# Kernel optimization log

Measured on AMD Instinct MI355X. Metric: run time of the kernel, lower is better.

Reference implementation:

```python
import jax, jax.numpy as jnp
import numpy as np

VOCAB = 32000
HIDDEN = 2048
NLAYERS = 6
BATCH = 512


def setup_inputs() -> dict:
    key = jax.random.key(0)
    k1, k2, k3, k4 = jax.random.split(key, 4)
    state = jax.random.normal(k1, (BATCH, HIDDEN), dtype=jnp.float32)
    token = jax.random.randint(k2, (BATCH,), 0, VOCAB, dtype=jnp.int32)
    ih = jax.random.normal(k3, (NLAYERS, VOCAB, HIDDEN), dtype=jnp.float32) * 0.02
    hh = jax.random.normal(k4, (NLAYERS, HIDDEN, HIDDEN), dtype=jnp.float32) * 0.02
    return {"state": state, "token": token, "ih": ih, "hh": hh}


def reference(state, token, ih, hh):
    # Per layer: state = tanh(state + (state @ hh[i]) * ih[i][token])
    n_layers = ih.shape[0]
    for i in range(n_layers):
        gate = ih[i][token]                  # [B, H] embedding gather
        state = jnp.tanh(state + jnp.matmul(state, hh[i]) * gate)
    return state
```

## Files before the change

kernel.cpp:

```cpp
#include <hip/hip_runtime.h>
#include <hip/hip_bf16.h>
#include <cstdint>
#include <cstddef>

#define VOCAB 32000
#define HIDDEN 2048
#define NLAYERS 6
#define BATCH 512

#define BM 64
#define BN 64
#define BK 64
#define SPLITK 4
#define KC (HIDDEN / SPLITK)
#define NT (KC / BK)
#define GEMM_BLOCKS 1024
#define TRANS_BLOCKS 1024
#define CVT_BLOCKS 1024

typedef __attribute__((ext_vector_type(8))) short bf16x8;
typedef __attribute__((ext_vector_type(4))) float f32x4;

__device__ __forceinline__ unsigned short f2bf(float f) {
  unsigned u = __builtin_bit_cast(unsigned, f);
  u += 0x7fffu + ((u >> 16) & 1u);
  return (unsigned short)(u >> 16);
}

__device__ __forceinline__ float bf2f(unsigned short h) {
  return __builtin_bit_cast(float, (unsigned)h << 16);
}

__device__ __forceinline__ float tanh_fast(float x) {
  x = fminf(15.f, fmaxf(-15.f, x));
  float e = __expf(2.f * x);
  return (e - 1.f) / (e + 1.f);
}

__device__ __forceinline__ void gload_lds16(const void* g, void* l) {
  __builtin_amdgcn_global_load_lds(
      (const __attribute__((address_space(1))) void*)g,
      (__attribute__((address_space(3))) void*)l, 16, 0, 0);
}

__device__ __forceinline__ void transpose_tile(const float* __restrict__ src_layer,
                                               unsigned short* __restrict__ dst_layer,
                                               int n0, int k0, int t,
                                               unsigned short (*tile)[72]) {
  const float* src = src_layer + (size_t)k0 * HIDDEN + n0;
  const int cr = t >> 4;
  const int cc = (t & 15) * 4;
#pragma unroll
  for (int p = 0; p < 4; ++p) {
    const int r = p * 16 + cr;
    float4 v = *(const float4*)(src + (size_t)r * HIDDEN + cc);
    tile[r][cc + 0] = f2bf(v.x);
    tile[r][cc + 1] = f2bf(v.y);
    tile[r][cc + 2] = f2bf(v.z);
    tile[r][cc + 3] = f2bf(v.w);
  }
  __syncthreads();
  const int nl = t >> 2;
  const int kk = (t & 3) * 16;
  unsigned short tmp[16] __attribute__((aligned(16)));
#pragma unroll
  for (int j = 0; j < 16; ++j) tmp[j] = tile[kk + j][nl];
  unsigned short* dst = dst_layer + (size_t)(n0 + nl) * HIDDEN + k0 + kk;
  *(uint4*)(dst) = *(const uint4*)(tmp);
  *(uint4*)(dst + 8) = *(const uint4*)(tmp + 8);
}

__global__ __launch_bounds__(256) void k_prep0(const float* __restrict__ hh0,
                                               unsigned short* __restrict__ bt0,
                                               const float* __restrict__ state,
                                               unsigned short* __restrict__ stb) {
  __shared__ unsigned short tile[64][72];
  const int wg = blockIdx.x;
  const int t = threadIdx.x;
  if (wg < TRANS_BLOCKS) {
    transpose_tile(hh0, bt0, (wg & 31) * 64, (wg >> 5) * 64, t, tile);
    return;
  }
  const int i = ((wg - TRANS_BLOCKS) * 256 + t) * 4;
  float4 v = *(const float4*)(state + i);
  union { unsigned short h[4]; uint2 u; } o;
  o.h[0] = f2bf(v.x); o.h[1] = f2bf(v.y); o.h[2] = f2bf(v.z); o.h[3] = f2bf(v.w);
  *(uint2*)(stb + i) = o.u;
}

__global__ __launch_bounds__(256, 4) void k_gemm_trans(
    const unsigned short* __restrict__ A, const unsigned short* __restrict__ Bt,
    unsigned short* __restrict__ part,
    const float* __restrict__ hhNext, unsigned short* __restrict__ btNext) {
  __shared__ __attribute__((aligned(16))) unsigned char smem[32768];
  const int t = threadIdx.x;
  const int wg = blockIdx.x;

  if (wg >= GEMM_BLOCKS) {
    const int tn = wg - GEMM_BLOCKS;
    transpose_tile(hhNext, btNext, (tn & 31) * 64, (tn >> 5) * 64, t,
                   (unsigned short(*)[72])smem);
    return;
  }

  unsigned short (*As)[BM][BK] = (unsigned short(*)[BM][BK])smem;
  unsigned short (*Bs)[BN][BK] = (unsigned short(*)[BN][BK])(smem + 16384);

  const int xcd = wg & 7;
  const int idx = wg >> 3;
  const int n0 = (xcd * 4 + (idx & 3)) * BN;
  const int m0 = ((idx >> 2) & 7) * BM;
  const int kz = idx >> 5;
  const int kbase = kz * KC;
  const int lane = t & 63;
  const int wid = t >> 6;
  const int wm = (wid >> 1) * 32;
  const int wn = (wid & 1) * 32;

  f32x4 zero = {0.f, 0.f, 0.f, 0.f};
  f32x4 acc[2][2];
  acc[0][0] = zero; acc[0][1] = zero; acc[1][0] = zero; acc[1][1] = zero;

  const int r0 = t >> 3;
  const int sc = ((t & 7) ^ (r0 & 7)) * 8;
  const unsigned short* gA = A + (size_t)(m0 + r0) * HIDDEN + kbase + sc;
  const unsigned short* gB = Bt + (size_t)(n0 + r0) * HIDDEN + kbase + sc;
  char* lA = (char*)smem + wid * 1024;
  char* lB = (char*)smem + 16384 + wid * 1024;

#define STAGE(buf, kt)                                          \
  do {                                                          \
    const int ko = (kt)*BK;                                     \
    gload_lds16(gA + ko, lA + (buf)*8192);                      \
    gload_lds16(gA + 32 * HIDDEN + ko, lA + (buf)*8192 + 4096); \
    gload_lds16(gB + ko, lB + (buf)*8192);                      \
    gload_lds16(gB + 32 * HIDDEN + ko, lB + (buf)*8192 + 4096); \
  } while (0)

  const int row_a0 = wm + (lane & 15);
  const int row_a1 = row_a0 + 16;
  const int row_b0 = wn + (lane & 15);
  const int row_b1 = row_b0 + 16;
  const int q = lane >> 4;

#define COMPUTE(buf)                                                                    \
  do {                                                                                  \
    _Pragma("unroll") for (int ks = 0; ks < 2; ++ks) {                                  \
      const int cnk = ks * 4 + q;                                                       \
      bf16x8 a0 = *(const bf16x8*)&As[buf][row_a0][(cnk ^ (row_a0 & 7)) * 8];           \
      bf16x8 a1 = *(const bf16x8*)&As[buf][row_a1][(cnk ^ (row_a1 & 7)) * 8];           \
      bf16x8 b0 = *(const bf16x8*)&Bs[buf][row_b0][(cnk ^ (row_b0 & 7)) * 8];           \
      bf16x8 b1 = *(const bf16x8*)&Bs[buf][row_b1][(cnk ^ (row_b1 & 7)) * 8];           \
      acc[0][0] = __builtin_amdgcn_mfma_f32_16x16x32_bf16(a0, b0, acc[0][0], 0, 0, 0);  \
      acc[0][1] = __builtin_amdgcn_mfma_f32_16x16x32_bf16(a0, b1, acc[0][1], 0, 0, 0);  \
      acc[1][0] = __builtin_amdgcn_mfma_f32_16x16x32_bf16(a1, b0, acc[1][0], 0, 0, 0);  \
      acc[1][1] = __builtin_amdgcn_mfma_f32_16x16x32_bf16(a1, b1, acc[1][1], 0, 0, 0);  \
    }                                                                                   \
  } while (0)

  STAGE(0, 0);
  for (int kt = 0; kt < NT; ++kt) {
    const int buf = kt & 1;
    if (kt + 1 < NT) {
      STAGE(buf ^ 1, kt + 1);
      asm volatile("s_waitcnt vmcnt(4)" ::: "memory");
    } else {
      asm volatile("s_waitcnt vmcnt(0)" ::: "memory");
    }
    __builtin_amdgcn_s_barrier();
    COMPUTE(buf);
    asm volatile("s_waitcnt lgkmcnt(0)" ::: "memory");
    __builtin_amdgcn_s_barrier();
  }

  unsigned short* p = part + (size_t)kz * ((size_t)BATCH * HIDDEN);
  const int rb = m0 + wm + (q << 2);
  const int cb = n0 + wn + (lane & 15);
#pragma unroll
  for (int fm = 0; fm < 2; ++fm)
#pragma unroll
    for (int fn = 0; fn < 2; ++fn)
#pragma unroll
      for (int j = 0; j < 4; ++j)
        p[(size_t)(rb + fm * 16 + j) * HIDDEN + cb + fn * 16] = f2bf(acc[fm][fn][j]);
}

__global__ __launch_bounds__(256) void k_reduce(const unsigned short* __restrict__ part,
                                                const float* __restrict__ prevf,
                                                unsigned short* __restrict__ stb,
                                                const float* __restrict__ ihl,
                                                const int* __restrict__ token,
                                                float* __restrict__ outf) {
  const int idx = (blockIdx.x * 256 + threadIdx.x) * 4;
  const int m = idx >> 11;
  const int n = idx & 2047;
  const size_t MN = (size_t)BATCH * HIDDEN;
  float s[4] = {0.f, 0.f, 0.f, 0.f};
#pragma unroll
  for (int kz = 0; kz < SPLITK; ++kz) {
    union { uint2 u; unsigned short h[4]; } v;
    v.u = *(const uint2*)(part + kz * MN + idx);
#pragma unroll
    for (int j = 0; j < 4; ++j) s[j] += bf2f(v.h[j]);
  }
  float pv[4];
  if (prevf) {
    float4 p4 = *(const float4*)(prevf + idx);
    pv[0] = p4.x; pv[1] = p4.y; pv[2] = p4.z; pv[3] = p4.w;
  } else {
    union { uint2 u; unsigned short h[4]; } p2;
    p2.u = *(const uint2*)(stb + idx);
#pragma unroll
    for (int j = 0; j < 4; ++j) pv[j] = bf2f(p2.h[j]);
  }
  const int tok = token[m];
  float4 g = *(const float4*)(ihl + (size_t)tok * HIDDEN + n);
  float r[4];
  r[0] = tanh_fast(pv[0] + s[0] * g.x);
  r[1] = tanh_fast(pv[1] + s[1] * g.y);
  r[2] = tanh_fast(pv[2] + s[2] * g.z);
  r[3] = tanh_fast(pv[3] + s[3] * g.w);
  if (outf) {
    float4 o4 = {r[0], r[1], r[2], r[3]};
    *(float4*)(outf + idx) = o4;
  } else {
    union { unsigned short h[4]; uint2 u; } o;
    o.h[0] = f2bf(r[0]); o.h[1] = f2bf(r[1]); o.h[2] = f2bf(r[2]); o.h[3] = f2bf(r[3]);
    *(uint2*)(stb + idx) = o.u;
  }
}

extern "C" void kernel_launch(void* const* d_in, const int* in_sizes, int n_in,
                              void* d_out, int out_size, void* d_ws, size_t ws_size,
                              hipStream_t stream) {
  const float* state = (const float*)d_in[0];
  const int* token = (const int*)d_in[1];
  const float* ih = (const float*)d_in[2];
  const float* hh = (const float*)d_in[3];
  float* out = (float*)d_out;

  char* ws = (char*)d_ws;
  unsigned short* bt = (unsigned short*)ws;
  size_t off = (size_t)NLAYERS * HIDDEN * HIDDEN * 2;
  unsigned short* stb = (unsigned short*)(ws + off);
  off += (size_t)BATCH * HIDDEN * 2;
  unsigned short* part = (unsigned short*)(ws + off);

  k_prep0<<<dim3(TRANS_BLOCKS + CVT_BLOCKS), 256, 0, stream>>>(hh, bt, state, stb);

  for (int l = 0; l < NLAYERS; ++l) {
    const bool last = (l == NLAYERS - 1);
    const int nblocks = GEMM_BLOCKS + (last ? 0 : TRANS_BLOCKS);
    k_gemm_trans<<<dim3(nblocks), 256, 0, stream>>>(
        stb, bt + (size_t)l * HIDDEN * HIDDEN, part,
        last ? nullptr : hh + (size_t)(l + 1) * HIDDEN * HIDDEN,
        last ? nullptr : bt + (size_t)(l + 1) * HIDDEN * HIDDEN);
    k_reduce<<<dim3((BATCH * HIDDEN) / 1024), 256, 0, stream>>>(
        part, l == 0 ? state : nullptr, stb,
        ih + (size_t)l * VOCAB * HIDDEN, token, last ? out : nullptr);
  }
}
```

Baseline: 110.6 us.

## Enlarge GEMM M-tile, double split-K, and load B fragments directly into registers

The GEMM tile grows to 128 rows with split-K raised from 4 to 8, keeping 1024 blocks. Each wave now computes a 64x32 sub-tile. The B operand no longer goes through shared memory: each lane loads its MFMA fragments straight from global memory into registers, double-buffered alongside the A staging. The K loop is fully unrolled by hand. This is meant to cut LDS traffic and barrier work per MFMA and raise A-tile reuse, but it doubles the partial-sum buffers the reduce kernel must write and read. It also assumes the partial buffer is large enough for 8 slices.

```diff
diff --git a/kernel.cpp b/kernel.cpp
--- a/kernel.cpp
+++ b/kernel.cpp
@@ -8,15 +8,16 @@
 #define NLAYERS 6
 #define BATCH 512
 
-#define BM 64
+#define BM 128
 #define BN 64
 #define BK 64
-#define SPLITK 4
+#define SPLITK 8
 #define KC (HIDDEN / SPLITK)
 #define NT (KC / BK)
 #define GEMM_BLOCKS 1024
 #define TRANS_BLOCKS 1024
 #define CVT_BLOCKS 1024
+#define MN ((size_t)BATCH * HIDDEN)
 
 typedef __attribute__((ext_vector_type(8))) short bf16x8;
 typedef __attribute__((ext_vector_type(4))) float f32x4;
@@ -103,81 +104,98 @@
     return;
   }
 
-  unsigned short (*As)[BM][BK] = (unsigned short(*)[BM][BK])smem;
-  unsigned short (*Bs)[BN][BK] = (unsigned short(*)[BN][BK])(smem + 16384);
-
   const int xcd = wg & 7;
   const int idx = wg >> 3;
   const int n0 = (xcd * 4 + (idx & 3)) * BN;
-  const int m0 = ((idx >> 2) & 7) * BM;
-  const int kz = idx >> 5;
+  const int m0 = ((idx >> 2) & 3) * BM;
+  const int kz = idx >> 4;
   const int kbase = kz * KC;
   const int lane = t & 63;
   const int wid = t >> 6;
-  const int wm = (wid >> 1) * 32;
+  const int wm = (wid >> 1) * 64;
   const int wn = (wid & 1) * 32;
+  const int q = lane >> 4;
 
   f32x4 zero = {0.f, 0.f, 0.f, 0.f};
-  f32x4 acc[2][2];
-  acc[0][0] = zero; acc[0][1] = zero; acc[1][0] = zero; acc[1][1] = zero;
+  f32x4 acc[4][2];
+#pragma unroll
+  for (int i = 0; i < 4; ++i) { acc[i][0] = zero; acc[i][1] = zero; }
 
   const int r0 = t >> 3;
   const int sc = ((t & 7) ^ (r0 & 7)) * 8;
   const unsigned short* gA = A + (size_t)(m0 + r0) * HIDDEN + kbase + sc;
-  const unsigned short* gB = Bt + (size_t)(n0 + r0) * HIDDEN + kbase + sc;
   char* lA = (char*)smem + wid * 1024;
-  char* lB = (char*)smem + 16384 + wid * 1024;
-
-#define STAGE(buf, kt)                                          \
-  do {                                                          \
-    const int ko = (kt)*BK;                                     \
-    gload_lds16(gA + ko, lA + (buf)*8192);                      \
-    gload_lds16(gA + 32 * HIDDEN + ko, lA + (buf)*8192 + 4096); \
-    gload_lds16(gB + ko, lB + (buf)*8192);                      \
-    gload_lds16(gB + 32 * HIDDEN + ko, lB + (buf)*8192 + 4096); \
+  unsigned short (*As)[BM][BK] = (unsigned short(*)[BM][BK])smem;
+
+#define STAGE_A(buf, kt)                                          \
+  do {                                                            \
+    const int ko = (kt)*BK;                                       \
+    gload_lds16(gA + ko, lA + (buf)*16384);                       \
+    gload_lds16(gA + 32 * HIDDEN + ko, lA + (buf)*16384 + 4096);  \
+    gload_lds16(gA + 64 * HIDDEN + ko, lA + (buf)*16384 + 8192);  \
+    gload_lds16(gA + 96 * HIDDEN + ko, lA + (buf)*16384 + 12288); \
   } while (0)
 
-  const int row_a0 = wm + (lane & 15);
-  const int row_a1 = row_a0 + 16;
-  const int row_b0 = wn + (lane & 15);
-  const int row_b1 = row_b0 + 16;
-  const int q = lane >> 4;
-
-#define COMPUTE(buf)                                                                    \
-  do {                                                                                  \
-    _Pragma("unroll") for (int ks = 0; ks < 2; ++ks) {                                  \
-      const int cnk = ks * 4 + q;                                                       \
-      bf16x8 a0 = *(const bf16x8*)&As[buf][row_a0][(cnk ^ (row_a0 & 7)) * 8];           \
-      bf16x8 a1 = *(const bf16x8*)&As[buf][row_a1][(cnk ^ (row_a1 & 7)) * 8];           \
-      bf16x8 b0 = *(const bf16x8*)&Bs[buf][row_b0][(cnk ^ (row_b0 & 7)) * 8];           \
-      bf16x8 b1 = *(const bf16x8*)&Bs[buf][row_b1][(cnk ^ (row_b1 & 7)) * 8];           \
-      acc[0][0] = __builtin_amdgcn_mfma_f32_16x16x32_bf16(a0, b0, acc[0][0], 0, 0, 0);  \
-      acc[0][1] = __builtin_amdgcn_mfma_f32_16x16x32_bf16(a0, b1, acc[0][1], 0, 0, 0);  \
-      acc[1][0] = __builtin_amdgcn_mfma_f32_16x16x32_bf16(a1, b0, acc[1][0], 0, 0, 0);  \
-      acc[1][1] = __builtin_amdgcn_mfma_f32_16x16x32_bf16(a1, b1, acc[1][1], 0, 0, 0);  \
-    }                                                                                   \
+  const unsigned short* gB =
+      Bt + (size_t)(n0 + wn + (lane & 15)) * HIDDEN + kbase + q * 8;
+
+#define B_LOAD(dst, kt)                                       \
+  do {                                                        \
+    const int ko = (kt)*BK;                                   \
+    dst[0][0] = *(const bf16x8*)(gB + ko);                    \
+    dst[0][1] = *(const bf16x8*)(gB + 16 * HIDDEN + ko);      \
+    dst[1][0] = *(const bf16x8*)(gB + ko + 32);               \
+    dst[1][1] = *(const bf16x8*)(gB + 16 * HIDDEN + ko + 32); \
   } while (0)
 
-  STAGE(0, 0);
-  for (int kt = 0; kt < NT; ++kt) {
-    const int buf = kt & 1;
-    if (kt + 1 < NT) {
-      STAGE(buf ^ 1, kt + 1);
-      asm volatile("s_waitcnt vmcnt(4)" ::: "memory");
-    } else {
-      asm volatile("s_waitcnt vmcnt(0)" ::: "memory");
-    }
-    __builtin_amdgcn_s_barrier();
-    COMPUTE(buf);
-    asm volatile("s_waitcnt lgkmcnt(0)" ::: "memory");
-    __builtin_amdgcn_s_barrier();
-  }
-
-  unsigned short* p = part + (size_t)kz * ((size_t)BATCH * HIDDEN);
+#define COMPUTE(buf, b)                                                              \
+  do {                                                                               \
+    _Pragma("unroll") for (int ks = 0; ks < 2; ++ks) {                               \
+      _Pragma("unroll") for (int fm = 0; fm < 4; ++fm) {                             \
+        const int ra = wm + (lane & 15) + fm * 16;                                   \
+        bf16x8 a = *(const bf16x8*)&As[buf][ra][((ks * 4 + q) ^ (lane & 7)) * 8];    \
+        acc[fm][0] =                                                                 \
+            __builtin_amdgcn_mfma_f32_16x16x32_bf16(a, b[0 + ks][0], acc[fm][0], 0, 0, 0); \
+        acc[fm][1] =                                                                 \
+            __builtin_amdgcn_mfma_f32_16x16x32_bf16(a, b[0 + ks][1], acc[fm][1], 0, 0, 0); \
+      }                                                                              \
+    }                                                                                \
+  } while (0)
+
+  bf16x8 bA[2][2], bB[2][2];
+  B_LOAD(bA, 0);
+  STAGE_A(0, 0);
+
+  STAGE_A(1, 1); B_LOAD(bB, 1);
+  asm volatile("s_waitcnt vmcnt(8)" ::: "memory");
+  __builtin_amdgcn_s_barrier();
+  COMPUTE(0, bA);
+  asm volatile("s_waitcnt lgkmcnt(0)" ::: "memory");
+  __builtin_amdgcn_s_barrier();
+
+  STAGE_A(0, 2); B_LOAD(bA, 2);
+  asm volatile("s_waitcnt vmcnt(8)" ::: "memory");
+  __builtin_amdgcn_s_barrier();
+  COMPUTE(1, bB);
+  asm volatile("s_waitcnt lgkmcnt(0)" ::: "memory");
+  __builtin_amdgcn_s_barrier();
+
+  STAGE_A(1, 3); B_LOAD(bB, 3);
+  asm volatile("s_waitcnt vmcnt(8)" ::: "memory");
+  __builtin_amdgcn_s_barrier();
+  COMPUTE(0, bA);
+  asm volatile("s_waitcnt lgkmcnt(0)" ::: "memory");
+  __builtin_amdgcn_s_barrier();
+
+  asm volatile("s_waitcnt vmcnt(0)" ::: "memory");
+  __builtin_amdgcn_s_barrier();
+  COMPUTE(1, bB);
+
+  unsigned short* p = part + (size_t)kz * MN;
   const int rb = m0 + wm + (q << 2);
   const int cb = n0 + wn + (lane & 15);
 #pragma unroll
-  for (int fm = 0; fm < 2; ++fm)
+  for (int fm = 0; fm < 4; ++fm)
 #pragma unroll
     for (int fn = 0; fn < 2; ++fn)
 #pragma unroll
@@ -194,7 +212,6 @@
   const int idx = (blockIdx.x * 256 + threadIdx.x) * 4;
   const int m = idx >> 11;
   const int n = idx & 2047;
-  const size_t MN = (size_t)BATCH * HIDDEN;
   float s[4] = {0.f, 0.f, 0.f, 0.f};
 #pragma unroll
   for (int kz = 0; kz < SPLITK; ++kz) {
```

Result: slower. 143.9 us (+30.1%).
